# Kernel optimization log

Measured on AMD Instinct MI355X. Metric: run time of the kernel, lower is better.

## Reference

```python
import jax, jax.numpy as jnp
import numpy as np


def _lyndon_indices(c, d):
    """All Lyndon words of length <= d over alphabet {0..c-1} via Duval's algorithm,
    mapped to flat indices into the flattened signature (levels 1..d concatenated,
    first letter most significant within each level). Static numpy computation."""
    words = []
    w = [-1]
    while w:
        w[-1] += 1
        words.append(tuple(w))
        m = len(w)
        while len(w) < d:
            w.append(w[len(w) - m])
        while w and w[-1] == c - 1:
            w.pop()
    words.sort(key=lambda t: (len(t), t))  # group by word length, lexicographic within
    offsets = np.concatenate([[0], np.cumsum([c ** k for k in range(1, d + 1)])])
    idx = []
    for word in words:
        pos = 0
        for letter in word:
            pos = pos * c + letter
        idx.append(int(offsets[len(word) - 1]) + pos)
    return np.asarray(idx, dtype=np.int64)


def _split_levels(sig, c, d):
    levels, start = [], 0
    for k in range(1, d + 1):
        n = c ** k
        levels.append(sig[:, start:start + n])  # (B, c^k)
        start += n
    return levels


def _mul_by_S(P, S, d):
    """Graded product P (x) S in the truncated tensor algebra (zero scalar parts).
    P[i], S[i] are level-(i+1) components of shape (B, c^(i+1)) or None."""
    B = S[0].shape[0]
    out = [None] * d
    for m in range(d):  # output level m+1
        acc = None
        for i in range(m):  # P level i+1 combines with S level m-i
            if P[i] is None:
                continue
            t = jnp.einsum('bi,bj->bij', P[i], S[m - 1 - i]).reshape(B, -1)
            acc = t if acc is None else acc + t
        out[m] = acc
    return out


def _log_signature_flat(sig, c, d):
    """log(1 + S) truncated at depth d, flattened levels 1..d."""
    S = _split_levels(sig, c, d)
    L = list(S)  # n=1 term (coefficient +1)
    P = S
    for n in range(2, d + 1):
        P = _mul_by_S(P, S, d)  # P = S^{(x) n}, levels < n are None
        coef = ((-1.0) ** (n + 1)) / n
        for k in range(d):
            if P[k] is not None:
                L[k] = L[k] + coef * P[k]
    return jnp.concatenate(L, axis=1)


def setup_inputs() -> dict:
    key = jax.random.key(0)
    channels, depth, batch = 8, 6, 64
    width = sum(channels ** k for k in range(1, depth + 1))  # 299592
    signature = jax.random.normal(key, (batch, width), dtype=jnp.float32) * 0.1
    return {"signature": signature, "channels": channels, "depth": depth}


def reference(signature, channels, depth):
    idx = jnp.asarray(_lyndon_indices(channels, depth))
    log_sig = _log_signature_flat(signature, channels, depth)  # (B, width)
    return log_sig[:, idx]  # Lyndon-word coefficients ('words' mode)
```

## Files before the change

### kernel.cpp

```cpp
#include <hip/hip_runtime.h>

#define NWIDTH 299592
#define NOUT   51360

typedef unsigned long long ull;
typedef unsigned short u16;

__device__ const int g_B2[8] = {8, 15, 21, 26, 30, 33, 35, 36};
__device__ const int g_B3[8] = {36, 92, 134, 164, 184, 196, 202, 204};
__device__ const int g_B4[8] = {204, 624, 897, 1062, 1152, 1194, 1209, 1212};
__device__ const int g_B5[8] = {1212, 4404, 6210, 7140, 7560, 7716, 7758, 7764};
__device__ const int g_C6[8] = {0, 24052, 35861, 41016, 42926, 43480, 43587, 43596};
__device__ const int g_uj1[16] = {0,0,0,0,0,0, 1,1,1,1, 2,2, 3, 4, 5, 6};
__device__ const int g_ur0[16] = {0, 4009, 8018, 12027, 16036, 20044,
                                  24052, 27005, 29957, 32909,
                                  35861, 38439, 41016, 42926, 43480, 43587};
__device__ const int g_ur1[16] = {4009, 8018, 12027, 16036, 20044, 24052,
                                  27005, 29957, 32909, 35861,
                                  38439, 41016, 42926, 43480, 43587, 43596};
__device__ const int g_ualg[16] = {1,0,0,0,0,0, 1,0,0,0, 1,0, 1, 1, 1, 1};

__device__ __forceinline__ bool is_lyndon6(unsigned p) {
  const unsigned mask = (1u << 18) - 1u;
#pragma unroll
  for (int k = 1; k < 6; ++k) {
    unsigned rot = ((p << (3 * k)) & mask) | (p >> (18 - 3 * k));
    if (p >= rot) return false;
  }
  return true;
}
__device__ __forceinline__ bool is_lyndon(unsigned p, int n) {
  const unsigned nb = 3u * (unsigned)n;
  const unsigned mask = (1u << nb) - 1u;
  for (int k = 1; k < n; ++k) {
    unsigned rot = ((p << (3 * k)) & mask) | (p >> (nb - 3 * k));
    if (p >= rot) return false;
  }
  return true;
}

__global__ __launch_bounds__(1024) void lyndon_prep(u16* __restrict__ pos16) {
  __shared__ int wsum[16];
  const int tid = threadIdx.x, lane = tid & 63, wv = tid >> 6;
  const int j = blockIdx.x;
  const unsigned pb = ((unsigned)j << 15) | ((unsigned)tid << 5);
  unsigned lm = 0;
  int c = 0;
  for (int i = 0; i < 32; ++i)
    if (is_lyndon6(pb | (unsigned)i)) { lm |= 1u << i; ++c; }
  int pref = c;
  for (int d = 1; d < 64; d <<= 1) { int t = __shfl_up(pref, d); if (lane >= d) pref += t; }
  if (lane == 63) wsum[wv] = pref;
  __syncthreads();
  int base = 0;
  for (int i = 0; i < wv; ++i) base += wsum[i];
  int ex = g_C6[j] + base + pref - c;
  unsigned m = lm;
  const int p0 = tid << 5;
  while (m) {
    const int bit = __builtin_ctz(m);
    pos16[ex++] = (u16)(p0 + bit);
    m &= m - 1;
  }
}

#define L_S3  0
#define L_S2  512
#define L_S1  576
#define L_A2  584
#define L_A3  592
#define L_A4  656
#define L_W2  1168
#define L_W3  1176
#define L_W4  1240
#define L_W4i 1752
#define L_W5i 1760
#define L_A5  1768
#define L_PL  5864
#define L_TOT 7872

__global__ __launch_bounds__(512)
void logsig_fused(const float* __restrict__ sig,
                  const u16* __restrict__ pos16,
                  float* __restrict__ out) {
  __shared__ __align__(16) float sm[L_TOT];
  int* W4i = (int*)(sm + L_W4i);
  int* W5i = (int*)(sm + L_W5i);
  u16* PL  = (u16*)(sm + L_PL);

  const int tid = threadIdx.x, lane = tid & 63, wv = tid >> 6;
  const int bid = blockIdx.x;
  const int xcd = bid & 7;
  const int rr  = bid >> 3;
  const int b   = xcd * 8 + (rr >> 4);
  const int u   = rr & 15;
  const int j1  = g_uj1[u];
  const bool isalg = g_ualg[u] != 0;
  const int r0 = g_ur0[u], r1 = g_ur1[u];
  const int cnt = r1 - r0;

  const float* __restrict__ S   = sig + (size_t)b * NWIDTH;
  const float* __restrict__ S4g = S + 584;
  const float* __restrict__ S5g = S + 4680;
  const float* __restrict__ S6j = S + 37448 + (size_t)j1 * 32768;
  float* __restrict__ outb = out + (size_t)b * NOUT;

  const float p1 = S[j1];
  const float c2 = -0.5f, c3 = 1.f / 3.f, c4 = -0.25f, c5 = 0.2f, c6 = -1.f / 6.f;
  const float c2p1 = c2 * p1;
  const float c3p1 = c3 * p1;
  const int q4 = tid << 2;

  sm[L_S3 + tid] = S[72 + tid];
  if (tid < 64) sm[L_S2 + tid] = S[8 + tid];
  if (tid < 8)  sm[L_S1 + tid] = S[tid];
  for (int i = tid; i < cnt; i += 512) PL[i] = pos16[r0 + i];
  const float s4p = S4g[j1 * 512 + tid];
  float p5[8];
  {
    float4 va = *(const float4*)(S5g + j1 * 4096 + q4);
    float4 vb = *(const float4*)(S5g + j1 * 4096 + 2048 + q4);
    p5[0] = va.x; p5[1] = va.y; p5[2] = va.z; p5[3] = va.w;
    p5[4] = vb.x; p5[5] = vb.y; p5[6] = vb.z; p5[7] = vb.w;
  }
  float4 s4qa, s4qb;
  s4qa = *(const float4*)(S4g + q4);
  s4qb = *(const float4*)(S4g + 2048 + q4);

  ull m4 = 0;
  unsigned fm5a = 0, fm5b = 0;
  int exA = 0, exB = 0;
  if (isalg) {
    bool f4 = is_lyndon(((unsigned)j1 << 9) | (unsigned)tid, 4);
    m4 = __ballot(f4);
    if (lane == 0) W4i[wv] = __popcll(m4);
    int c5a = 0, c5b = 0;
#pragma unroll
    for (int e = 0; e < 4; ++e) {
      if (is_lyndon(((unsigned)j1 << 12) | (unsigned)(q4 + e), 5)) { fm5a |= 1u << e; ++c5a; }
      if (is_lyndon(((unsigned)j1 << 12) | (unsigned)(2048 + q4 + e), 5)) { fm5b |= 1u << e; ++c5b; }
    }
    int prefpk = c5a | (c5b << 16);
    for (int d = 1; d < 64; d <<= 1) { int t = __shfl_up(prefpk, d); if (lane >= d) prefpk += t; }
    if (lane == 63) W5i[wv] = prefpk;
    exA = (prefpk & 0xffff) - c5a;
    exB = (prefpk >> 16) - c5b;
  }
  __syncthreads();

  {
    const int x = tid;
    const float s1_4 = sm[L_S1 + (x & 7)];
    const float s1_3 = sm[L_S1 + ((x >> 3) & 7)];
    const float s1_2 = sm[L_S1 + (x >> 6)];
    const float s3p  = sm[L_S3 + j1 * 64 + (x >> 3)];
    const float s2p  = sm[L_S2 + j1 * 8 + (x >> 6)];
    const float w4_2 = s3p * s1_4 + s2p * sm[L_S2 + (x & 63)] + p1 * sm[L_S3 + x];
    const float w4_3 = (s2p * s1_3 + p1 * sm[L_S2 + (x >> 3)]) * s1_4
                     + p1 * s1_2 * sm[L_S2 + (x & 63)];
    const float w4_4 = p1 * s1_2 * s1_3 * s1_4;
    sm[L_A4 + x] = c2 * s4p + c3 * w4_2 + c4 * w4_3 + c5 * w4_4;
    sm[L_W4 + x] = c3 * s4p + c4 * w4_2 + c5 * w4_3 + c6 * w4_4;
  }
  if (tid < 64) {
    const int y = tid;
    const float w3_2 = sm[L_S2 + j1 * 8 + (y >> 3)] * sm[L_S1 + (y & 7)]
                     + p1 * sm[L_S2 + y];
    const float w3_3 = p1 * sm[L_S1 + (y >> 3)] * sm[L_S1 + (y & 7)];
    const float s3py = sm[L_S3 + j1 * 64 + y];
    sm[L_A3 + y] = c2 * s3py + c3 * w3_2 + c4 * w3_3;
    sm[L_W3 + y] = c3 * s3py + c4 * w3_2 + c5 * w3_3;
  }
  if (tid < 8) {
    const int z = tid;
    const float s2pz = sm[L_S2 + j1 * 8 + z];
    const float s1z  = sm[L_S1 + z];
    sm[L_A2 + z] = c2 * s2pz + c3 * p1 * s1z;
    sm[L_W2 + z] = c3 * s2pz + c4 * p1 * s1z;
  }
  __syncthreads();

  const float s1t = sm[L_S1 + (tid & 7)];
  float s1q4[4];
#pragma unroll
  for (int e = 0; e < 4; ++e) s1q4[e] = sm[L_S1 + ((tid & 1) << 2) + e];

  float l5a[4], l5b[4];
  {
    const float W4a = sm[L_W4 + (tid >> 1)],       W4b = sm[L_W4 + 256 + (tid >> 1)];
    const float A4a = sm[L_A4 + (tid >> 1)],       A4b = sm[L_A4 + 256 + (tid >> 1)];
    const float W3a = sm[L_W3 + (tid >> 4)],       W3b = sm[L_W3 + 32 + (tid >> 4)];
    const float A3a = sm[L_A3 + (tid >> 4)],       A3b = sm[L_A3 + 32 + (tid >> 4)];
    const float W2a = sm[L_W2 + (tid >> 7)],       W2b = sm[L_W2 + 4 + (tid >> 7)];
    const float A2a = sm[L_A2 + (tid >> 7)],       A2b = sm[L_A2 + 4 + (tid >> 7)];
    const float4 s2v = *(const float4*)(sm + L_S2 + (q4 & 63));
    const float4 s3v = *(const float4*)(sm + L_S3 + (q4 & 511));
    const float s2q[4] = {s2v.x, s2v.y, s2v.z, s2v.w};
    const float s3q[4] = {s3v.x, s3v.y, s3v.z, s3v.w};
    const float s4a[4] = {s4qa.x, s4qa.y, s4qa.z, s4qa.w};
    const float s4b[4] = {s4qb.x, s4qb.y, s4qb.z, s4qb.w};
    float a5A[4], a5B[4];
#pragma unroll
    for (int e = 0; e < 4; ++e) {
      a5A[e] = c2 * p5[e]     + W4a * s1q4[e] + W3a * s2q[e] + W2a * s3q[e] + c3p1 * s4a[e];
      a5B[e] = c2 * p5[4 + e] + W4b * s1q4[e] + W3b * s2q[e] + W2b * s3q[e] + c3p1 * s4b[e];
      l5a[e] = p5[e]     + A4a * s1q4[e] + A3a * s2q[e] + A2a * s3q[e] + c2p1 * s4a[e];
      l5b[e] = p5[4 + e] + A4b * s1q4[e] + A3b * s2q[e] + A2b * s3q[e] + c2p1 * s4b[e];
    }
    *(float4*)(sm + L_A5 + q4)        = make_float4(a5A[0], a5A[1], a5A[2], a5A[3]);
    *(float4*)(sm + L_A5 + 2048 + q4) = make_float4(a5B[0], a5B[1], a5B[2], a5B[3]);
  }

  if (isalg) {
    float l2v = 0.f, l3v = 0.f;
    if (tid < 8)
      l2v = sm[L_S2 + j1 * 8 + tid] + c2p1 * s1t;
    if (tid < 64)
      l3v = sm[L_S3 + j1 * 64 + tid] + sm[L_A2 + (tid >> 3)] * s1t
          + c2p1 * sm[L_S2 + tid];
    const float l4v = s4p + sm[L_A3 + (tid >> 3)] * s1t
                    + sm[L_A2 + (tid >> 6)] * sm[L_S2 + (tid & 63)]
                    + c2p1 * sm[L_S3 + tid];
    if (tid == 0) {
      outb[j1] = p1;
      if (j1 == 0) outb[7] = sm[L_S1 + 7];
    }
    if (tid < 8 && tid > j1) outb[g_B2[j1] + tid - j1 - 1] = l2v;
    if (tid < 64) {
      bool f3 = is_lyndon(((unsigned)j1 << 6) | (unsigned)tid, 3);
      ull m3 = __ballot(f3);
      if (f3) outb[g_B3[j1] + __popcll(m3 & ((1ull << lane) - 1ull))] = l3v;
    }
    {
      int base = 0;
      for (int i = 0; i < wv; ++i) base += W4i[i];
      if ((m4 >> lane) & 1ull)
        outb[g_B4[j1] + base + __popcll(m4 & ((1ull << lane) - 1ull))] = l4v;
    }
    {
      int baseA = 0, baseB = 0, totalA = 0;
#pragma unroll
      for (int i = 0; i < 8; ++i) {
        int w = W5i[i];
        totalA += w & 0xffff;
        if (i < wv) { baseA += w & 0xffff; baseB += w >> 16; }
      }
      int slotA = g_B5[j1] + baseA + exA;
      int slotB = g_B5[j1] + totalA + baseB + exB;
#pragma unroll
      for (int e = 0; e < 4; ++e)
        if ((fm5a >> e) & 1u) outb[slotA++] = l5a[e];
#pragma unroll
      for (int e = 0; e < 4; ++e)
        if ((fm5b >> e) & 1u) outb[slotB++] = l5b[e];
    }
  }
  __syncthreads();

  float* __restrict__ outr = outb + 7764 + r0;
  for (int i = tid; i < cnt; i += 512) {
    const int pl = PL[i];
    float v = S6j[pl]
            + sm[L_A5 + (pl >> 3)] * sm[L_S1 + (pl & 7)]
            + sm[L_A4 + (pl >> 6)] * sm[L_S2 + (pl & 63)]
            + sm[L_A3 + (pl >> 9)] * sm[L_S3 + (pl & 511)]
            + sm[L_A2 + (pl >> 12)] * S4g[pl & 4095]
            + c2p1 * S5g[pl];
    outr[i] = v;
  }
}


extern "C" void kernel_launch(void* const* d_in, const int* in_sizes, int n_in,
                              void* d_out, int out_size, void* d_ws, size_t ws_size,
                              hipStream_t stream) {
  const float* sig = (const float*)d_in[0];
  float* out = (float*)d_out;
  u16* pos16 = (u16*)d_ws;

  lyndon_prep<<<7, 1024, 0, stream>>>(pos16);
  logsig_fused<<<1024, 512, 0, stream>>>(sig, pos16, out);
}
```

Measured before the change: 40.29 us.

## Merge Lyndon prep into main kernel via cooperative launch with grid sync

```diff
diff --git a/kernel.cpp b/kernel.cpp
--- a/kernel.cpp
+++ b/kernel.cpp
@@ -1,4 +1,7 @@
 #include <hip/hip_runtime.h>
+#include <hip/hip_cooperative_groups.h>
+
+namespace cg = cooperative_groups;
 
 #define NWIDTH 299592
 #define NOUT   51360
@@ -37,6 +40,251 @@
     if (p >= rot) return false;
   }
   return true;
+}
+
+#define L_S3  0
+#define L_S2  512
+#define L_S1  576
+#define L_A2  584
+#define L_A3  592
+#define L_A4  656
+#define L_W2  1168
+#define L_W3  1176
+#define L_W4  1240
+#define L_W4i 1752
+#define L_W5i 1760
+#define L_A5  1768
+#define L_PL  5864
+#define L_TOT 7872
+
+template <int COOP>
+__device__ __forceinline__ void logsig_body(const float* __restrict__ sig,
+                                            u16* __restrict__ pos16,
+                                            float* __restrict__ out,
+                                            float* sm) {
+  int* W4i = (int*)(sm + L_W4i);
+  int* W5i = (int*)(sm + L_W5i);
+  u16* PL  = (u16*)(sm + L_PL);
+
+  const int tid = threadIdx.x, lane = tid & 63, wv = tid >> 6;
+  const int bid = blockIdx.x;
+  const int xcd = bid & 7;
+  const int rr  = bid >> 3;
+  const int b   = xcd * 8 + (rr >> 4);
+  const int u   = rr & 15;
+  const int j1  = g_uj1[u];
+  const bool isalg = g_ualg[u] != 0;
+  const int r0 = g_ur0[u], r1 = g_ur1[u];
+  const int cnt = r1 - r0;
+
+  if (COOP && bid < 7) {
+    const int j = bid;
+    const unsigned pb = ((unsigned)j << 15) | ((unsigned)tid << 6);
+    ull m = 0;
+    int c = 0;
+    for (int i = 0; i < 64; ++i)
+      if (is_lyndon6(pb | (unsigned)i)) { m |= (1ull << i); ++c; }
+    int pref = c;
+    for (int d = 1; d < 64; d <<= 1) { int t = __shfl_up(pref, d); if (lane >= d) pref += t; }
+    if (lane == 63) W4i[wv] = pref;
+    __syncthreads();
+    int base = 0;
+    for (int i = 0; i < wv; ++i) base += W4i[i];
+    int ex = g_C6[j] + base + pref - c;
+    while (m) {
+      const int bit = __builtin_ctzll(m);
+      pos16[ex++] = (u16)((tid << 6) + bit);
+      m &= m - 1;
+    }
+    __threadfence();
+    __syncthreads();
+  }
+
+  const float* __restrict__ S   = sig + (size_t)b * NWIDTH;
+  const float* __restrict__ S4g = S + 584;
+  const float* __restrict__ S5g = S + 4680;
+  const float* __restrict__ S6j = S + 37448 + (size_t)j1 * 32768;
+  float* __restrict__ outb = out + (size_t)b * NOUT;
+
+  const float p1 = S[j1];
+  const float c2 = -0.5f, c3 = 1.f / 3.f, c4 = -0.25f, c5 = 0.2f, c6 = -1.f / 6.f;
+  const float c2p1 = c2 * p1;
+  const float c3p1 = c3 * p1;
+  const int q4 = tid << 2;
+
+  sm[L_S3 + tid] = S[72 + tid];
+  if (tid < 64) sm[L_S2 + tid] = S[8 + tid];
+  if (tid < 8)  sm[L_S1 + tid] = S[tid];
+  if (!COOP) {
+    for (int i = tid; i < cnt; i += 512) PL[i] = pos16[r0 + i];
+  }
+  const float s4p = S4g[j1 * 512 + tid];
+  float p5[8];
+  {
+    float4 va = *(const float4*)(S5g + j1 * 4096 + q4);
+    float4 vb = *(const float4*)(S5g + j1 * 4096 + 2048 + q4);
+    p5[0] = va.x; p5[1] = va.y; p5[2] = va.z; p5[3] = va.w;
+    p5[4] = vb.x; p5[5] = vb.y; p5[6] = vb.z; p5[7] = vb.w;
+  }
+  float4 s4qa, s4qb;
+  s4qa = *(const float4*)(S4g + q4);
+  s4qb = *(const float4*)(S4g + 2048 + q4);
+
+  ull m4 = 0;
+  unsigned fm5a = 0, fm5b = 0;
+  int exA = 0, exB = 0;
+  if (isalg) {
+    bool f4 = is_lyndon(((unsigned)j1 << 9) | (unsigned)tid, 4);
+    m4 = __ballot(f4);
+    if (lane == 0) W4i[wv] = __popcll(m4);
+    int c5a = 0, c5b = 0;
+#pragma unroll
+    for (int e = 0; e < 4; ++e) {
+      if (is_lyndon(((unsigned)j1 << 12) | (unsigned)(q4 + e), 5)) { fm5a |= 1u << e; ++c5a; }
+      if (is_lyndon(((unsigned)j1 << 12) | (unsigned)(2048 + q4 + e), 5)) { fm5b |= 1u << e; ++c5b; }
+    }
+    int prefpk = c5a | (c5b << 16);
+    for (int d = 1; d < 64; d <<= 1) { int t = __shfl_up(prefpk, d); if (lane >= d) prefpk += t; }
+    if (lane == 63) W5i[wv] = prefpk;
+    exA = (prefpk & 0xffff) - c5a;
+    exB = (prefpk >> 16) - c5b;
+  }
+
+  if (COOP) {
+    cg::this_grid().sync();
+    for (int i = tid; i < cnt; i += 512) PL[i] = pos16[r0 + i];
+  } else {
+    __syncthreads();
+  }
+
+  {
+    const int x = tid;
+    const float s1_4 = sm[L_S1 + (x & 7)];
+    const float s1_3 = sm[L_S1 + ((x >> 3) & 7)];
+    const float s1_2 = sm[L_S1 + (x >> 6)];
+    const float s3p  = sm[L_S3 + j1 * 64 + (x >> 3)];
+    const float s2p  = sm[L_S2 + j1 * 8 + (x >> 6)];
+    const float w4_2 = s3p * s1_4 + s2p * sm[L_S2 + (x & 63)] + p1 * sm[L_S3 + x];
+    const float w4_3 = (s2p * s1_3 + p1 * sm[L_S2 + (x >> 3)]) * s1_4
+                     + p1 * s1_2 * sm[L_S2 + (x & 63)];
+    const float w4_4 = p1 * s1_2 * s1_3 * s1_4;
+    sm[L_A4 + x] = c2 * s4p + c3 * w4_2 + c4 * w4_3 + c5 * w4_4;
+    sm[L_W4 + x] = c3 * s4p + c4 * w4_2 + c5 * w4_3 + c6 * w4_4;
+  }
+  if (tid < 64) {
+    const int y = tid;
+    const float w3_2 = sm[L_S2 + j1 * 8 + (y >> 3)] * sm[L_S1 + (y & 7)]
+                     + p1 * sm[L_S2 + y];
+    const float w3_3 = p1 * sm[L_S1 + (y >> 3)] * sm[L_S1 + (y & 7)];
+    const float s3py = sm[L_S3 + j1 * 64 + y];
+    sm[L_A3 + y] = c2 * s3py + c3 * w3_2 + c4 * w3_3;
+    sm[L_W3 + y] = c3 * s3py + c4 * w3_2 + c5 * w3_3;
+  }
+  if (tid < 8) {
+    const int z = tid;
+    const float s2pz = sm[L_S2 + j1 * 8 + z];
+    const float s1z  = sm[L_S1 + z];
+    sm[L_A2 + z] = c2 * s2pz + c3 * p1 * s1z;
+    sm[L_W2 + z] = c3 * s2pz + c4 * p1 * s1z;
+  }
+  __syncthreads();
+
+  const float s1t = sm[L_S1 + (tid & 7)];
+  float s1q4[4];
+#pragma unroll
+  for (int e = 0; e < 4; ++e) s1q4[e] = sm[L_S1 + ((tid & 1) << 2) + e];
+
+  float l5a[4], l5b[4];
+  {
+    const float W4a = sm[L_W4 + (tid >> 1)],       W4b = sm[L_W4 + 256 + (tid >> 1)];
+    const float A4a = sm[L_A4 + (tid >> 1)],       A4b = sm[L_A4 + 256 + (tid >> 1)];
+    const float W3a = sm[L_W3 + (tid >> 4)],       W3b = sm[L_W3 + 32 + (tid >> 4)];
+    const float A3a = sm[L_A3 + (tid >> 4)],       A3b = sm[L_A3 + 32 + (tid >> 4)];
+    const float W2a = sm[L_W2 + (tid >> 7)],       W2b = sm[L_W2 + 4 + (tid >> 7)];
+    const float A2a = sm[L_A2 + (tid >> 7)],       A2b = sm[L_A2 + 4 + (tid >> 7)];
+    const float4 s2v = *(const float4*)(sm + L_S2 + (q4 & 63));
+    const float4 s3v = *(const float4*)(sm + L_S3 + (q4 & 511));
+    const float s2q[4] = {s2v.x, s2v.y, s2v.z, s2v.w};
+    const float s3q[4] = {s3v.x, s3v.y, s3v.z, s3v.w};
+    const float s4a[4] = {s4qa.x, s4qa.y, s4qa.z, s4qa.w};
+    const float s4b[4] = {s4qb.x, s4qb.y, s4qb.z, s4qb.w};
+    float a5A[4], a5B[4];
+#pragma unroll
+    for (int e = 0; e < 4; ++e) {
+      a5A[e] = c2 * p5[e]     + W4a * s1q4[e] + W3a * s2q[e] + W2a * s3q[e] + c3p1 * s4a[e];
+      a5B[e] = c2 * p5[4 + e] + W4b * s1q4[e] + W3b * s2q[e] + W2b * s3q[e] + c3p1 * s4b[e];
+      l5a[e] = p5[e]     + A4a * s1q4[e] + A3a * s2q[e] + A2a * s3q[e] + c2p1 * s4a[e];
+      l5b[e] = p5[4 + e] + A4b * s1q4[e] + A3b * s2q[e] + A2b * s3q[e] + c2p1 * s4b[e];
+    }
+    *(float4*)(sm + L_A5 + q4)        = make_float4(a5A[0], a5A[1], a5A[2], a5A[3]);
+    *(float4*)(sm + L_A5 + 2048 + q4) = make_float4(a5B[0], a5B[1], a5B[2], a5B[3]);
+  }
+
+  if (isalg) {
+    float l2v = 0.f, l3v = 0.f;
+    if (tid < 8)
+      l2v = sm[L_S2 + j1 * 8 + tid] + c2p1 * s1t;
+    if (tid < 64)
+      l3v = sm[L_S3 + j1 * 64 + tid] + sm[L_A2 + (tid >> 3)] * s1t
+          + c2p1 * sm[L_S2 + tid];
+    const float l4v = s4p + sm[L_A3 + (tid >> 3)] * s1t
+                    + sm[L_A2 + (tid >> 6)] * sm[L_S2 + (tid & 63)]
+                    + c2p1 * sm[L_S3 + tid];
+    if (tid == 0) {
+      outb[j1] = p1;
+      if (j1 == 0) outb[7] = sm[L_S1 + 7];
+    }
+    if (tid < 8 && tid > j1) outb[g_B2[j1] + tid - j1 - 1] = l2v;
+    if (tid < 64) {
+      bool f3 = is_lyndon(((unsigned)j1 << 6) | (unsigned)tid, 3);
+      ull m3 = __ballot(f3);
+      if (f3) outb[g_B3[j1] + __popcll(m3 & ((1ull << lane) - 1ull))] = l3v;
+    }
+    {
+      int base = 0;
+      for (int i = 0; i < wv; ++i) base += W4i[i];
+      if ((m4 >> lane) & 1ull)
+        outb[g_B4[j1] + base + __popcll(m4 & ((1ull << lane) - 1ull))] = l4v;
+    }
+    {
+      int baseA = 0, baseB = 0, totalA = 0;
+#pragma unroll
+      for (int i = 0; i < 8; ++i) {
+        int w = W5i[i];
+        totalA += w & 0xffff;
+        if (i < wv) { baseA += w & 0xffff; baseB += w >> 16; }
+      }
+      int slotA = g_B5[j1] + baseA + exA;
+      int slotB = g_B5[j1] + totalA + baseB + exB;
+#pragma unroll
+      for (int e = 0; e < 4; ++e)
+        if ((fm5a >> e) & 1u) outb[slotA++] = l5a[e];
+#pragma unroll
+      for (int e = 0; e < 4; ++e)
+        if ((fm5b >> e) & 1u) outb[slotB++] = l5b[e];
+    }
+  }
+  __syncthreads();
+
+  float* __restrict__ outr = outb + 7764 + r0;
+  for (int i = tid; i < cnt; i += 512) {
+    const int pl = PL[i];
+    float v = S6j[pl]
+            + sm[L_A5 + (pl >> 3)] * sm[L_S1 + (pl & 7)]
+            + sm[L_A4 + (pl >> 6)] * sm[L_S2 + (pl & 63)]
+            + sm[L_A3 + (pl >> 9)] * sm[L_S3 + (pl & 511)]
+            + sm[L_A2 + (pl >> 12)] * S4g[pl & 4095]
+            + c2p1 * S5g[pl];
+    outr[i] = v;
+  }
+}
+
+__global__ __launch_bounds__(512, 8)
+void logsig_coop(const float* __restrict__ sig,
+                 u16* __restrict__ pos16,
+                 float* __restrict__ out) {
+  __shared__ __align__(16) float sm[L_TOT];
+  logsig_body<1>(sig, pos16, out, sm);
 }
 
 __global__ __launch_bounds__(1024) void lyndon_prep(u16* __restrict__ pos16) {
@@ -64,210 +312,12 @@
   }
 }
 
-#define L_S3  0
-#define L_S2  512
-#define L_S1  576
-#define L_A2  584
-#define L_A3  592
-#define L_A4  656
-#define L_W2  1168
-#define L_W3  1176
-#define L_W4  1240
-#define L_W4i 1752
-#define L_W5i 1760
-#define L_A5  1768
-#define L_PL  5864
-#define L_TOT 7872
-
 __global__ __launch_bounds__(512)
 void logsig_fused(const float* __restrict__ sig,
-                  const u16* __restrict__ pos16,
+                  u16* __restrict__ pos16,
                   float* __restrict__ out) {
   __shared__ __align__(16) float sm[L_TOT];
-  int* W4i = (int*)(sm + L_W4i);
-  int* W5i = (int*)(sm + L_W5i);
-  u16* PL  = (u16*)(sm + L_PL);
-
-  const int tid = threadIdx.x, lane = tid & 63, wv = tid >> 6;
-  const int bid = blockIdx.x;
-  const int xcd = bid & 7;
-  const int rr  = bid >> 3;
-  const int b   = xcd * 8 + (rr >> 4);
-  const int u   = rr & 15;
-  const int j1  = g_uj1[u];
-  const bool isalg = g_ualg[u] != 0;
-  const int r0 = g_ur0[u], r1 = g_ur1[u];
-  const int cnt = r1 - r0;
-
-  const float* __restrict__ S   = sig + (size_t)b * NWIDTH;
-  const float* __restrict__ S4g = S + 584;
-  const float* __restrict__ S5g = S + 4680;
-  const float* __restrict__ S6j = S + 37448 + (size_t)j1 * 32768;
-  float* __restrict__ outb = out + (size_t)b * NOUT;
-
-  const float p1 = S[j1];
-  const float c2 = -0.5f, c3 = 1.f / 3.f, c4 = -0.25f, c5 = 0.2f, c6 = -1.f / 6.f;
-  const float c2p1 = c2 * p1;
-  const float c3p1 = c3 * p1;
-  const int q4 = tid << 2;
-
-  sm[L_S3 + tid] = S[72 + tid];
-  if (tid < 64) sm[L_S2 + tid] = S[8 + tid];
-  if (tid < 8)  sm[L_S1 + tid] = S[tid];
-  for (int i = tid; i < cnt; i += 512) PL[i] = pos16[r0 + i];
-  const float s4p = S4g[j1 * 512 + tid];
-  float p5[8];
-  {
-    float4 va = *(const float4*)(S5g + j1 * 4096 + q4);
-    float4 vb = *(const float4*)(S5g + j1 * 4096 + 2048 + q4);
-    p5[0] = va.x; p5[1] = va.y; p5[2] = va.z; p5[3] = va.w;
-    p5[4] = vb.x; p5[5] = vb.y; p5[6] = vb.z; p5[7] = vb.w;
-  }
-  float4 s4qa, s4qb;
-  s4qa = *(const float4*)(S4g + q4);
-  s4qb = *(const float4*)(S4g + 2048 + q4);
-
-  ull m4 = 0;
-  unsigned fm5a = 0, fm5b = 0;
-  int exA = 0, exB = 0;
-  if (isalg) {
-    bool f4 = is_lyndon(((unsigned)j1 << 9) | (unsigned)tid, 4);
-    m4 = __ballot(f4);
-    if (lane == 0) W4i[wv] = __popcll(m4);
-    int c5a = 0, c5b = 0;
-#pragma unroll
-    for (int e = 0; e < 4; ++e) {
-      if (is_lyndon(((unsigned)j1 << 12) | (unsigned)(q4 + e), 5)) { fm5a |= 1u << e; ++c5a; }
-      if (is_lyndon(((unsigned)j1 << 12) | (unsigned)(2048 + q4 + e), 5)) { fm5b |= 1u << e; ++c5b; }
-    }
-    int prefpk = c5a | (c5b << 16);
-    for (int d = 1; d < 64; d <<= 1) { int t = __shfl_up(prefpk, d); if (lane >= d) prefpk += t; }
-    if (lane == 63) W5i[wv] = prefpk;
-    exA = (prefpk & 0xffff) - c5a;
-    exB = (prefpk >> 16) - c5b;
-  }
-  __syncthreads();
-
-  {
-    const int x = tid;
-    const float s1_4 = sm[L_S1 + (x & 7)];
-    const float s1_3 = sm[L_S1 + ((x >> 3) & 7)];
-    const float s1_2 = sm[L_S1 + (x >> 6)];
-    const float s3p  = sm[L_S3 + j1 * 64 + (x >> 3)];
-    const float s2p  = sm[L_S2 + j1 * 8 + (x >> 6)];
-    const float w4_2 = s3p * s1_4 + s2p * sm[L_S2 + (x & 63)] + p1 * sm[L_S3 + x];
-    const float w4_3 = (s2p * s1_3 + p1 * sm[L_S2 + (x >> 3)]) * s1_4
-                     + p1 * s1_2 * sm[L_S2 + (x & 63)];
-    const float w4_4 = p1 * s1_2 * s1_3 * s1_4;
-    sm[L_A4 + x] = c2 * s4p + c3 * w4_2 + c4 * w4_3 + c5 * w4_4;
-    sm[L_W4 + x] = c3 * s4p + c4 * w4_2 + c5 * w4_3 + c6 * w4_4;
-  }
-  if (tid < 64) {
-    const int y = tid;
-    const float w3_2 = sm[L_S2 + j1 * 8 + (y >> 3)] * sm[L_S1 + (y & 7)]
-                     + p1 * sm[L_S2 + y];
-    const float w3_3 = p1 * sm[L_S1 + (y >> 3)] * sm[L_S1 + (y & 7)];
-    const float s3py = sm[L_S3 + j1 * 64 + y];
-    sm[L_A3 + y] = c2 * s3py + c3 * w3_2 + c4 * w3_3;
-    sm[L_W3 + y] = c3 * s3py + c4 * w3_2 + c5 * w3_3;
-  }
-  if (tid < 8) {
-    const int z = tid;
-    const float s2pz = sm[L_S2 + j1 * 8 + z];
-    const float s1z  = sm[L_S1 + z];
-    sm[L_A2 + z] = c2 * s2pz + c3 * p1 * s1z;
-    sm[L_W2 + z] = c3 * s2pz + c4 * p1 * s1z;
-  }
-  __syncthreads();
-
-  const float s1t = sm[L_S1 + (tid & 7)];
-  float s1q4[4];
-#pragma unroll
-  for (int e = 0; e < 4; ++e) s1q4[e] = sm[L_S1 + ((tid & 1) << 2) + e];
-
-  float l5a[4], l5b[4];
-  {
-    const float W4a = sm[L_W4 + (tid >> 1)],       W4b = sm[L_W4 + 256 + (tid >> 1)];
-    const float A4a = sm[L_A4 + (tid >> 1)],       A4b = sm[L_A4 + 256 + (tid >> 1)];
-    const float W3a = sm[L_W3 + (tid >> 4)],       W3b = sm[L_W3 + 32 + (tid >> 4)];
-    const float A3a = sm[L_A3 + (tid >> 4)],       A3b = sm[L_A3 + 32 + (tid >> 4)];
-    const float W2a = sm[L_W2 + (tid >> 7)],       W2b = sm[L_W2 + 4 + (tid >> 7)];
-    const float A2a = sm[L_A2 + (tid >> 7)],       A2b = sm[L_A2 + 4 + (tid >> 7)];
-    const float4 s2v = *(const float4*)(sm + L_S2 + (q4 & 63));
-    const float4 s3v = *(const float4*)(sm + L_S3 + (q4 & 511));
-    const float s2q[4] = {s2v.x, s2v.y, s2v.z, s2v.w};
-    const float s3q[4] = {s3v.x, s3v.y, s3v.z, s3v.w};
-    const float s4a[4] = {s4qa.x, s4qa.y, s4qa.z, s4qa.w};
-    const float s4b[4] = {s4qb.x, s4qb.y, s4qb.z, s4qb.w};
-    float a5A[4], a5B[4];
-#pragma unroll
-    for (int e = 0; e < 4; ++e) {
-      a5A[e] = c2 * p5[e]     + W4a * s1q4[e] + W3a * s2q[e] + W2a * s3q[e] + c3p1 * s4a[e];
-      a5B[e] = c2 * p5[4 + e] + W4b * s1q4[e] + W3b * s2q[e] + W2b * s3q[e] + c3p1 * s4b[e];
-      l5a[e] = p5[e]     + A4a * s1q4[e] + A3a * s2q[e] + A2a * s3q[e] + c2p1 * s4a[e];
-      l5b[e] = p5[4 + e] + A4b * s1q4[e] + A3b * s2q[e] + A2b * s3q[e] + c2p1 * s4b[e];
-    }
-    *(float4*)(sm + L_A5 + q4)        = make_float4(a5A[0], a5A[1], a5A[2], a5A[3]);
-    *(float4*)(sm + L_A5 + 2048 + q4) = make_float4(a5B[0], a5B[1], a5B[2], a5B[3]);
-  }
-
-  if (isalg) {
-    float l2v = 0.f, l3v = 0.f;
-    if (tid < 8)
-      l2v = sm[L_S2 + j1 * 8 + tid] + c2p1 * s1t;
-    if (tid < 64)
-      l3v = sm[L_S3 + j1 * 64 + tid] + sm[L_A2 + (tid >> 3)] * s1t
-          + c2p1 * sm[L_S2 + tid];
-    const float l4v = s4p + sm[L_A3 + (tid >> 3)] * s1t
-                    + sm[L_A2 + (tid >> 6)] * sm[L_S2 + (tid & 63)]
-                    + c2p1 * sm[L_S3 + tid];
-    if (tid == 0) {
-      outb[j1] = p1;
-      if (j1 == 0) outb[7] = sm[L_S1 + 7];
-    }
-    if (tid < 8 && tid > j1) outb[g_B2[j1] + tid - j1 - 1] = l2v;
-    if (tid < 64) {
-      bool f3 = is_lyndon(((unsigned)j1 << 6) | (unsigned)tid, 3);
-      ull m3 = __ballot(f3);
-      if (f3) outb[g_B3[j1] + __popcll(m3 & ((1ull << lane) - 1ull))] = l3v;
-    }
-    {
-      int base = 0;
-      for (int i = 0; i < wv; ++i) base += W4i[i];
-      if ((m4 >> lane) & 1ull)
-        outb[g_B4[j1] + base + __popcll(m4 & ((1ull << lane) - 1ull))] = l4v;
-    }
-    {
-      int baseA = 0, baseB = 0, totalA = 0;
-#pragma unroll
-      for (int i = 0; i < 8; ++i) {
-        int w = W5i[i];
-        totalA += w & 0xffff;
-        if (i < wv) { baseA += w & 0xffff; baseB += w >> 16; }
-      }
-      int slotA = g_B5[j1] + baseA + exA;
-      int slotB = g_B5[j1] + totalA + baseB + exB;
-#pragma unroll
-      for (int e = 0; e < 4; ++e)
-        if ((fm5a >> e) & 1u) outb[slotA++] = l5a[e];
-#pragma unroll
-      for (int e = 0; e < 4; ++e)
-        if ((fm5b >> e) & 1u) outb[slotB++] = l5b[e];
-    }
-  }
-  __syncthreads();
-
-  float* __restrict__ outr = outb + 7764 + r0;
-  for (int i = tid; i < cnt; i += 512) {
-    const int pl = PL[i];
-    float v = S6j[pl]
-            + sm[L_A5 + (pl >> 3)] * sm[L_S1 + (pl & 7)]
-            + sm[L_A4 + (pl >> 6)] * sm[L_S2 + (pl & 63)]
-            + sm[L_A3 + (pl >> 9)] * sm[L_S3 + (pl & 511)]
-            + sm[L_A2 + (pl >> 12)] * S4g[pl & 4095]
-            + c2p1 * S5g[pl];
-    outr[i] = v;
-  }
+  logsig_body<0>(sig, pos16, out, sm);
 }
 
 
@@ -278,6 +328,11 @@
   float* out = (float*)d_out;
   u16* pos16 = (u16*)d_ws;
 
-  lyndon_prep<<<7, 1024, 0, stream>>>(pos16);
-  logsig_fused<<<1024, 512, 0, stream>>>(sig, pos16, out);
-}
+  void* args[] = {(void*)&sig, (void*)&pos16, (void*)&out};
+  hipError_t e = hipLaunchCooperativeKernel((const void*)logsig_coop,
+                                            dim3(1024), dim3(512), args, 0, stream);
+  if (e != hipSuccess) {
+    lyndon_prep<<<7, 1024, 0, stream>>>(pos16);
+    logsig_fused<<<1024, 512, 0, stream>>>(sig, pos16, out);
+  }
+}
```

New measurement: 143.3 us. 3.56x slower.
